# Kernel tuning notes

Measured on AMD Instinct MI355X. Metric: run time of the kernel, lower is better.

Reference implementation:

```python
import math
import jax, jax.numpy as jnp
import numpy as np

IN_FEATURES = 4096
OUT_FEATURES = 4096
BLOCK_SIZE = 256
N_TOKENS = 8192


def _butterfly_layout(out_blocks, in_blocks, butterfly_size):
    # sum of log2(n) butterfly factors with all-ones 2x2 twiddles:
    # block (o, i) is active iff o == i or o == i ^ 2^k for some factor k
    log_n = int(math.log2(butterfly_size))
    idx = np.arange(butterfly_size)
    layout = np.zeros((butterfly_size, butterfly_size), dtype=bool)
    layout[idx, idx] = True
    for k in range(log_n):
        layout[idx ^ (1 << k), idx] = True
    if out_blocks > butterfly_size:
        layout = np.tile(layout, (out_blocks // butterfly_size, 1))
    if in_blocks > butterfly_size:
        layout = np.tile(layout, (1, in_blocks // butterfly_size))
    return layout


def _flat_indices(layout):
    # For each output block, flat indices into [num_in_blocks * active_blocks_per_input]
    # selecting which per-input weight blocks are summed (embedding_bag mode='sum').
    num_out, num_in = layout.shape
    abpi = int(layout.sum(0)[0])
    abpo = int(layout.sum(1)[0])
    rank = np.cumsum(layout, axis=0) - 1  # rank of output o among active outputs of input i
    o_idx, i_idx = np.nonzero(layout)     # row-major -> grouped by output block
    flat = i_idx * abpi + rank[o_idx, i_idx]
    return flat.reshape(num_out, abpo).astype(np.int32), abpi


def setup_inputs() -> dict:
    key = jax.random.key(0)
    k1, k2 = jax.random.split(key)
    in_blocks = IN_FEATURES // BLOCK_SIZE
    out_blocks = OUT_FEATURES // BLOCK_SIZE
    butterfly_size = min(IN_FEATURES, OUT_FEATURES) // BLOCK_SIZE  # 16
    layout = _butterfly_layout(out_blocks, in_blocks, butterfly_size)
    flat_idx, abpi = _flat_indices(layout)  # abpi = log2(16)+1 = 5
    std = math.sqrt(2.0 / (5 * min(IN_FEATURES, OUT_FEATURES)))
    weight = jax.random.normal(k1, (IN_FEATURES, abpi, BLOCK_SIZE), dtype=jnp.float32) * std
    x = jax.random.normal(k2, (N_TOKENS, IN_FEATURES), dtype=jnp.float32)
    return {"x": x, "weight": weight, "flat_indices": jnp.asarray(flat_idx)}


def reference(x, weight, flat_indices):
    # x: [B, in_features]; weight: [in_features, abpi, block_size]
    in_features, abpi, bs = weight.shape
    num_in = in_features // bs
    B = x.shape[0]
    xb = x.reshape(B, num_in, bs)                  # [B, g, k]
    w = weight.reshape(num_in, bs, abpi, bs)       # [g, k, a, o]
    # per-input-block partial output blocks: [g, a, B, o]
    blocks = jnp.einsum('bgk,gkao->gabo', xb, w)
    blocks = blocks.reshape(num_in * abpi, B, bs)
    # gather + sum active blocks per output block (embedding_bag mode='sum')
    out_blocks = blocks[flat_indices].sum(axis=1)  # [num_out_blocks, B, bs]
    out = jnp.transpose(out_blocks, (1, 0, 2)).reshape(B, -1)  # [B, out_features]
    return out
```

## Files before the change

kernel.cpp:

```cpp
#include <hip/hip_runtime.h>
#include <stdint.h>

#define N_TOK 8192
#define IN_F 4096
#define OUT_F 4096
#define BS 256
#define ABPI 5
#define NFLAT 80

typedef __attribute__((ext_vector_type(8))) short short8;
typedef __attribute__((ext_vector_type(4))) float floatx4;
typedef __attribute__((ext_vector_type(4))) unsigned short ushort4v;
typedef __attribute__((ext_vector_type(8))) unsigned short ushort8v;

__device__ __forceinline__ unsigned short f2bf(float f) {
  union { float f; unsigned int u; } v; v.f = f;
  unsigned int r = v.u + 0x7FFFu + ((v.u >> 16) & 1u);
  return (unsigned short)(r >> 16);
}

__device__ __forceinline__ void async16(const void* g, void* l) {
  __builtin_amdgcn_global_load_lds((const __attribute__((address_space(1))) void*)g,
                                   (__attribute__((address_space(3))) void*)l, 16, 0, 0);
}

__global__ void cvt_x_kernel(const float4* __restrict__ x, ushort8v* __restrict__ xb) {
  int idx = blockIdx.x * 256 + threadIdx.x;
  float4 a = x[idx * 2], b = x[idx * 2 + 1];
  ushort8v o;
  o[0] = f2bf(a.x); o[1] = f2bf(a.y); o[2] = f2bf(a.z); o[3] = f2bf(a.w);
  o[4] = f2bf(b.x); o[5] = f2bf(b.y); o[6] = f2bf(b.z); o[7] = f2bf(b.w);
  xb[idx] = o;
}

__global__ void cvt_w_kernel(const float* __restrict__ w, unsigned short* __restrict__ wt) {
  __shared__ unsigned short tile[64][68];
  int b = blockIdx.x;
  int fi = b >> 4;
  int t  = b & 15;
  int k0 = (t >> 2) * 64, o0 = (t & 3) * 64;
  int g = fi / ABPI, a = fi % ABPI;
  int tid = threadIdx.x;
  int tr = tid >> 4, tc = tid & 15;
  #pragma unroll
  for (int i = 0; i < 4; ++i) {
    int k = k0 + i * 16 + tr;
    const float* src = w + (size_t)(g * 256 + k) * (ABPI * BS) + a * BS + o0 + tc * 4;
    float4 v = *(const float4*)src;
    tile[tc * 4 + 0][i * 16 + tr] = f2bf(v.x);
    tile[tc * 4 + 1][i * 16 + tr] = f2bf(v.y);
    tile[tc * 4 + 2][i * 16 + tr] = f2bf(v.z);
    tile[tc * 4 + 3][i * 16 + tr] = f2bf(v.w);
  }
  __syncthreads();
  #pragma unroll
  for (int i = 0; i < 4; ++i) {
    int o = i * 16 + tr;
    unsigned short* dst = wt + (size_t)fi * (BS * BS) + (size_t)(o0 + o) * BS + k0 + tc * 4;
    *(ushort4v*)dst = *(const ushort4v*)&tile[o][tc * 4];
  }
}

__global__ __launch_bounds__(256, 2)
void bfly_gemm(const unsigned short* __restrict__ xb,
               const unsigned short* __restrict__ wt,
               const int* __restrict__ fidx,
               float* __restrict__ out)
{
  __shared__ __align__(16) short As[128 * 64];
  __shared__ __align__(16) short Bs[128 * 64];

  const int tid = threadIdx.x;
  const int bx  = blockIdx.x;
  const int ob  = bx >> 7;
  const int rem = bx & 127;
  const int m0  = (rem >> 1) * 128;
  const int nh  = rem & 1;
  const int n0g = ob * 256 + nh * 128;

  int wbase[ABPI], gcol[ABPI];
  #pragma unroll
  for (int s = 0; s < ABPI; ++s) {
    int fi = fidx[ob * ABPI + s];
    wbase[s] = fi * (BS * BS);
    gcol[s]  = (fi / ABPI) * BS;
  }

  const int sr = tid >> 3;
  const int sc = tid & 7;
  const int lc = sc ^ (sr & 7);
  const size_t aBase = (size_t)(m0 + sr) * IN_F + lc * 8;
  const int    bBase = (nh * 128 + sr) * BS + lc * 8;
  short* aDst = As + tid * 8;
  short* bDst = Bs + tid * 8;

  const int lane = tid & 63;
  const int wv   = tid >> 6;
  const int wm   = (wv & 1) * 64;
  const int wn   = (wv >> 1) * 64;
  const int lrow = lane & 15;
  const int quad = lane >> 4;

  floatx4 acc[4][4] = {};

  for (int c = 0; c < 20; ++c) {
    const int s  = c >> 2;
    const int kk = (c & 3) * 64;
    const unsigned short* aG = xb + aBase + gcol[s] + kk;
    const unsigned short* bG = wt + wbase[s] + bBase + kk;
    __syncthreads();
    #pragma unroll
    for (int i = 0; i < 4; ++i) {
      async16(aG + (size_t)i * 32 * IN_F, aDst + i * 2048);
      async16(bG + i * 32 * BS,           bDst + i * 2048);
    }
    __syncthreads();
    #pragma unroll
    for (int ks = 0; ks < 2; ++ks) {
      short8 af[4], bf[4];
      const int ch = ((ks * 4 + quad) ^ (lrow & 7)) * 8;
      #pragma unroll
      for (int mt = 0; mt < 4; ++mt)
        af[mt] = *(const short8*)(As + (wm + mt * 16 + lrow) * 64 + ch);
      #pragma unroll
      for (int nt = 0; nt < 4; ++nt)
        bf[nt] = *(const short8*)(Bs + (wn + nt * 16 + lrow) * 64 + ch);
      #pragma unroll
      for (int mt = 0; mt < 4; ++mt)
        #pragma unroll
        for (int nt = 0; nt < 4; ++nt)
          acc[mt][nt] = __builtin_amdgcn_mfma_f32_16x16x32_bf16(af[mt], bf[nt], acc[mt][nt], 0, 0, 0);
    }
  }

  #pragma unroll
  for (int mt = 0; mt < 4; ++mt) {
    const int rbase = m0 + wm + mt * 16 + quad * 4;
    #pragma unroll
    for (int nt = 0; nt < 4; ++nt) {
      const int col = n0g + wn + nt * 16 + lrow;
      float* po = out + (size_t)rbase * OUT_F + col;
      #pragma unroll
      for (int r = 0; r < 4; ++r)
        po[(size_t)r * OUT_F] = acc[mt][nt][r];
    }
  }
}

extern "C" void kernel_launch(void* const* d_in, const int* in_sizes, int n_in,
                              void* d_out, int out_size, void* d_ws, size_t ws_size,
                              hipStream_t stream) {
  const float* x  = (const float*)d_in[0];
  const float* w  = (const float*)d_in[1];
  const int* fidx = (const int*)d_in[2];
  float* out = (float*)d_out;

  unsigned short* xb = (unsigned short*)d_ws;
  unsigned short* wt = xb + (size_t)N_TOK * IN_F;

  cvt_x_kernel<<<(N_TOK * IN_F) / (8 * 256), 256, 0, stream>>>((const float4*)x, (ushort8v*)xb);
  cvt_w_kernel<<<NFLAT * 16, 256, 0, stream>>>(w, wt);
  bfly_gemm<<<16 * 64 * 2, 256, 0, stream>>>(xb, wt, fidx, out);
}
```

Before: 355.6 us.

## Rewrite butterfly GEMM with 256x128 tiles and triple-buffered async LDS pipeline

Replaces the 128x128 single-buffered GEMM loop with a 512-thread, 256x128 tile kernel. It uses three LDS buffers in dynamic shared memory, filled by global_load_lds. Each k-tile is split into two phases that interleave the next tile's loads with fragment reads and MFMA work, using explicit waitcnt, sched_barrier and setprio. The intent is to hide global load latency and raise data reuse per block. It also adds a block-index swizzle for L2 locality and readfirstlane on the gathered indices. The cost is roughly 147KB of LDS per block, which limits occupancy to one block per CU, plus fragile hand-managed synchronisation.

```diff
diff --git a/kernel.cpp b/kernel.cpp
--- a/kernel.cpp
+++ b/kernel.cpp
@@ -61,27 +61,114 @@
   }
 }
 
-__global__ __launch_bounds__(256, 2)
+
+#define BM 256
+#define BN 128
+#define BK 64
+#define ABYTES 32768
+#define BBYTES 16384
+#define BUFBYTES 49152
+#define SMEM_TOTAL 147456
+
+__device__ __forceinline__ void ld_frags(const char* Ab, const char* Bb,
+                                         int rA, int rB, int c0, int c1, int mbyte, bool rdB,
+                                         short8 (&af)[4][2], short8 (&bfr)[2][2]) {
+  #pragma unroll
+  for (int m = 0; m < 4; ++m) {
+    const char* p = Ab + rA + mbyte + m * 2048;
+    af[m][0] = *(const short8*)(p + c0);
+    af[m][1] = *(const short8*)(p + c1);
+  }
+  if (rdB) {
+    #pragma unroll
+    for (int n = 0; n < 2; ++n) {
+      const char* p = Bb + rB + n * 2048;
+      bfr[n][0] = *(const short8*)(p + c0);
+      bfr[n][1] = *(const short8*)(p + c1);
+    }
+  }
+}
+
+__device__ __forceinline__ void mma_frags(int mbase, const short8 (&af)[4][2],
+                                          const short8 (&bfr)[2][2], floatx4 (&acc)[8][2]) {
+  #pragma unroll
+  for (int m = 0; m < 4; ++m)
+    #pragma unroll
+    for (int n = 0; n < 2; ++n) {
+      acc[mbase + m][n] = __builtin_amdgcn_mfma_f32_16x16x32_bf16(af[m][0], bfr[n][0], acc[mbase + m][n], 0, 0, 0);
+      acc[mbase + m][n] = __builtin_amdgcn_mfma_f32_16x16x32_bf16(af[m][1], bfr[n][1], acc[mbase + m][n], 0, 0, 0);
+    }
+}
+
+#define STAGE_PH0(uA, uB, Adst, Bdst)              \
+  do {                                             \
+    async16(pA0 + (uA), (Adst)         + tid16);   \
+    async16(pA1 + (uA), (Adst) +  8192 + tid16);   \
+    async16(pB0 + (uB), (Bdst)         + tid16);   \
+  } while (0)
+#define STAGE_PH1(uA, uB, Adst, Bdst)              \
+  do {                                             \
+    async16(pA2 + (uA), (Adst) + 16384 + tid16);   \
+    async16(pA3 + (uA), (Adst) + 24576 + tid16);   \
+    async16(pB1 + (uB), (Bdst) +  8192 + tid16);   \
+  } while (0)
+
+#define KTILE(u, Ab, Bb, Asd, Bsd, DOSTAGE, LASTWAIT)                       \
+  do {                                                                      \
+    int uA = 0, uB = 0;                                                     \
+    if (DOSTAGE) { int su = (u) >> 2, ku = ((u) & 3) * 64;                  \
+                   uA = gcol[su] + ku; uB = wbase[su] + ku; }               \
+    ld_frags(Ab, Bb, rA, rB, c0, c1, 0, true, af, bfr);                     \
+    if (DOSTAGE) STAGE_PH0(uA, uB, Asd, Bsd);                               \
+    __builtin_amdgcn_s_barrier();                                           \
+    asm volatile("s_waitcnt lgkmcnt(0)" ::: "memory");                      \
+    __builtin_amdgcn_sched_barrier(0);                                      \
+    __builtin_amdgcn_s_setprio(1);                                          \
+    mma_frags(0, af, bfr, acc);                                             \
+    __builtin_amdgcn_s_setprio(0);                                          \
+    __builtin_amdgcn_s_barrier();                                           \
+    ld_frags(Ab, Bb, rA, rB, c0, c1, 8192, false, af, bfr);                 \
+    if (DOSTAGE) STAGE_PH1(uA, uB, Asd, Bsd);                               \
+    __builtin_amdgcn_s_barrier();                                           \
+    asm volatile("s_waitcnt lgkmcnt(0)" ::: "memory");                      \
+    __builtin_amdgcn_sched_barrier(0);                                      \
+    __builtin_amdgcn_s_setprio(1);                                          \
+    mma_frags(4, af, bfr, acc);                                             \
+    __builtin_amdgcn_s_setprio(0);                                          \
+    if (DOSTAGE)       { asm volatile("s_waitcnt vmcnt(6)" ::: "memory");   \
+                         __builtin_amdgcn_sched_barrier(0); }               \
+    else if (LASTWAIT) { asm volatile("s_waitcnt vmcnt(0)" ::: "memory");   \
+                         __builtin_amdgcn_sched_barrier(0); }               \
+    __builtin_amdgcn_s_barrier();                                           \
+  } while (0)
+
+__global__ __launch_bounds__(512, 2)
 void bfly_gemm(const unsigned short* __restrict__ xb,
                const unsigned short* __restrict__ wt,
                const int* __restrict__ fidx,
                float* __restrict__ out)
 {
-  __shared__ __align__(16) short As[128 * 64];
-  __shared__ __align__(16) short Bs[128 * 64];
+  extern __shared__ __align__(16) char smem[];
+  char* const b0A = smem;
+  char* const b0B = b0A + ABYTES;
+  char* const b1A = smem + BUFBYTES;
+  char* const b1B = b1A + ABYTES;
+  char* const b2A = smem + 2 * BUFBYTES;
+  char* const b2B = b2A + ABYTES;
 
   const int tid = threadIdx.x;
   const int bx  = blockIdx.x;
-  const int ob  = bx >> 7;
-  const int rem = bx & 127;
-  const int m0  = (rem >> 1) * 128;
-  const int nh  = rem & 1;
+  const int swz = (bx & 7) * 128 + (bx >> 3);
+  const int ob  = swz >> 6;
+  const int mt  = (swz >> 1) & 31;
+  const int nh  = swz & 1;
+  const int m0  = mt * BM;
   const int n0g = ob * 256 + nh * 128;
 
   int wbase[ABPI], gcol[ABPI];
   #pragma unroll
   for (int s = 0; s < ABPI; ++s) {
-    int fi = fidx[ob * ABPI + s];
+    int fi = __builtin_amdgcn_readfirstlane(fidx[ob * ABPI + s]);
     wbase[s] = fi * (BS * BS);
     gcol[s]  = (fi / ABPI) * BS;
   }
@@ -89,60 +176,60 @@
   const int sr = tid >> 3;
   const int sc = tid & 7;
   const int lc = sc ^ (sr & 7);
-  const size_t aBase = (size_t)(m0 + sr) * IN_F + lc * 8;
-  const int    bBase = (nh * 128 + sr) * BS + lc * 8;
-  short* aDst = As + tid * 8;
-  short* bDst = Bs + tid * 8;
+  const int tid16 = tid * 16;
+  const unsigned short* pA0 = xb + (size_t)(m0 +   0 + sr) * IN_F + lc * 8;
+  const unsigned short* pA1 = xb + (size_t)(m0 +  64 + sr) * IN_F + lc * 8;
+  const unsigned short* pA2 = xb + (size_t)(m0 + 128 + sr) * IN_F + lc * 8;
+  const unsigned short* pA3 = xb + (size_t)(m0 + 192 + sr) * IN_F + lc * 8;
+  const unsigned short* pB0 = wt + (nh * 128 +  0 + sr) * BS + lc * 8;
+  const unsigned short* pB1 = wt + (nh * 128 + 64 + sr) * BS + lc * 8;
 
   const int lane = tid & 63;
   const int wv   = tid >> 6;
-  const int wm   = (wv & 1) * 64;
-  const int wn   = (wv >> 1) * 64;
+  const int wm   = (wv >> 2) * 128;
+  const int wn   = (wv & 3) * 32;
   const int lrow = lane & 15;
   const int quad = lane >> 4;
-
-  floatx4 acc[4][4] = {};
-
-  for (int c = 0; c < 20; ++c) {
-    const int s  = c >> 2;
-    const int kk = (c & 3) * 64;
-    const unsigned short* aG = xb + aBase + gcol[s] + kk;
-    const unsigned short* bG = wt + wbase[s] + bBase + kk;
-    __syncthreads();
+  const int rA = (wm + lrow) * 128;
+  const int rB = (wn + lrow) * 128;
+  const int c0 = ((quad)     ^ (lrow & 7)) * 16;
+  const int c1 = ((quad + 4) ^ (lrow & 7)) * 16;
+
+  short8 af[4][2], bfr[2][2];
+  floatx4 acc[8][2] = {};
+
+  {
+    const int uA0 = gcol[0], uB0 = wbase[0];
+    STAGE_PH0(uA0, uB0, b0A, b0B);
+    STAGE_PH1(uA0, uB0, b0A, b0B);
+    __builtin_amdgcn_sched_barrier(0);
+    STAGE_PH0(uA0 + 64, uB0 + 64, b1A, b1B);
+    STAGE_PH1(uA0 + 64, uB0 + 64, b1A, b1B);
+    asm volatile("s_waitcnt vmcnt(6)" ::: "memory");
+    __builtin_amdgcn_sched_barrier(0);
+    __builtin_amdgcn_s_barrier();
+  }
+
+  #pragma unroll 1
+  for (int j = 0; j < 6; ++j) {
+    const int t = j * 3;
+    KTILE(t + 2, b0A, b0B, b2A, b2B, true, false);
+    KTILE(t + 3, b1A, b1B, b0A, b0B, true, false);
+    KTILE(t + 4, b2A, b2B, b1A, b1B, true, false);
+  }
+  KTILE(0, b0A, b0B, b0A, b0B, false, true);
+  KTILE(0, b1A, b1B, b0A, b0B, false, false);
+
+  #pragma unroll
+  for (int m = 0; m < 8; ++m) {
+    const int row = m0 + wm + m * 16 + quad * 4;
     #pragma unroll
-    for (int i = 0; i < 4; ++i) {
-      async16(aG + (size_t)i * 32 * IN_F, aDst + i * 2048);
-      async16(bG + i * 32 * BS,           bDst + i * 2048);
-    }
-    __syncthreads();
-    #pragma unroll
-    for (int ks = 0; ks < 2; ++ks) {
-      short8 af[4], bf[4];
-      const int ch = ((ks * 4 + quad) ^ (lrow & 7)) * 8;
-      #pragma unroll
-      for (int mt = 0; mt < 4; ++mt)
-        af[mt] = *(const short8*)(As + (wm + mt * 16 + lrow) * 64 + ch);
-      #pragma unroll
-      for (int nt = 0; nt < 4; ++nt)
-        bf[nt] = *(const short8*)(Bs + (wn + nt * 16 + lrow) * 64 + ch);
-      #pragma unroll
-      for (int mt = 0; mt < 4; ++mt)
-        #pragma unroll
-        for (int nt = 0; nt < 4; ++nt)
-          acc[mt][nt] = __builtin_amdgcn_mfma_f32_16x16x32_bf16(af[mt], bf[nt], acc[mt][nt], 0, 0, 0);
-    }
-  }
-
-  #pragma unroll
-  for (int mt = 0; mt < 4; ++mt) {
-    const int rbase = m0 + wm + mt * 16 + quad * 4;
-    #pragma unroll
-    for (int nt = 0; nt < 4; ++nt) {
-      const int col = n0g + wn + nt * 16 + lrow;
-      float* po = out + (size_t)rbase * OUT_F + col;
+    for (int n = 0; n < 2; ++n) {
+      const int col = n0g + wn + n * 16 + lrow;
+      float* po = out + (size_t)row * OUT_F + col;
       #pragma unroll
       for (int r = 0; r < 4; ++r)
-        po[(size_t)r * OUT_F] = acc[mt][nt][r];
+        po[(size_t)r * OUT_F] = acc[m][n][r];
     }
   }
 }
@@ -158,7 +245,14 @@
   unsigned short* xb = (unsigned short*)d_ws;
   unsigned short* wt = xb + (size_t)N_TOK * IN_F;
 
+  static int smem_set = 0;
+  if (!smem_set) {
+    hipFuncSetAttribute((const void*)bfly_gemm,
+                        hipFuncAttributeMaxDynamicSharedMemorySize, SMEM_TOTAL);
+    smem_set = 1;
+  }
+
   cvt_x_kernel<<<(N_TOK * IN_F) / (8 * 256), 256, 0, stream>>>((const float4*)x, (ushort8v*)xb);
   cvt_w_kernel<<<NFLAT * 16, 256, 0, stream>>>(w, wt);
-  bfly_gemm<<<16 * 64 * 2, 256, 0, stream>>>(xb, wt, fidx, out);
-}
+  bfly_gemm<<<16 * 32 * 2, 512, SMEM_TOTAL, stream>>>(xb, wt, fidx, out);
+}
```

New measurement: 333.3 us. 6.3% less time.

## Rewrite butterfly GEMM as 256x256 double-buffered, phase-interleaved MFMA kernel

Applied to the files above, without the earlier changes.

Replaces the 128x128 single-buffered GEMM with a 256x256 tile per 512-thread block. It double-buffers A and B in 128KB of dynamic LDS and splits each K tile into four phases that interleave async global-to-LDS loads with MFMA work, using explicit vmcnt waits and s_setprio. It also swizzles the block index for L2 locality and makes the weight-index loads wave-uniform with readfirstlane. The aim is to hide load latency and raise reuse per loaded byte. In exchange it uses far more registers and LDS, which limits occupancy, and the hand-tuned barrier and waitcnt scheme is fragile.

```diff
diff --git a/kernel.cpp b/kernel.cpp
--- a/kernel.cpp
+++ b/kernel.cpp
@@ -61,27 +61,117 @@
   }
 }
 
-__global__ __launch_bounds__(256, 2)
+
+#define BM 256
+#define BN 256
+#define BK 64
+#define ABYTES 32768
+#define BUFBYTES 65536
+#define SMEM_TOTAL 131072
+
+__device__ __forceinline__ void ld_half_A(const char* p, int c0, int c1, short8 (&af)[4][2]) {
+  #pragma unroll
+  for (int mt = 0; mt < 4; ++mt) {
+    const char* q = p + mt * 2048;
+    af[mt][0] = *(const short8*)(q + c0);
+    af[mt][1] = *(const short8*)(q + c1);
+  }
+}
+
+__device__ __forceinline__ void ld_pair_B(const char* p, int c0, int c1, short8 (&bf)[2][2]) {
+  #pragma unroll
+  for (int nt = 0; nt < 2; ++nt) {
+    const char* q = p + nt * 2048;
+    bf[nt][0] = *(const short8*)(q + c0);
+    bf[nt][1] = *(const short8*)(q + c1);
+  }
+}
+
+__device__ __forceinline__ void mma16(const short8 (&af)[4][2], const short8 (&bf)[2][2],
+                                      floatx4 (&acc)[8][4], int mb, int nb) {
+  #pragma unroll
+  for (int mt = 0; mt < 4; ++mt)
+    #pragma unroll
+    for (int nt = 0; nt < 2; ++nt) {
+      acc[mb + mt][nb + nt] =
+          __builtin_amdgcn_mfma_f32_16x16x32_bf16(af[mt][0], bf[nt][0], acc[mb + mt][nb + nt], 0, 0, 0);
+      acc[mb + mt][nb + nt] =
+          __builtin_amdgcn_mfma_f32_16x16x32_bf16(af[mt][1], bf[nt][1], acc[mb + mt][nb + nt], 0, 0, 0);
+    }
+}
+
+#define PH_OPEN                                            \
+  __builtin_amdgcn_s_barrier();                            \
+  asm volatile("s_waitcnt lgkmcnt(0)" ::: "memory");       \
+  __builtin_amdgcn_sched_barrier(0);                       \
+  __builtin_amdgcn_s_setprio(1)
+
+#define KTILE(tt, Ab, Bb, Asd, Bsd, DOSTAGE, LAST)                              \
+  do {                                                                          \
+    int uA = 0, uB = 0;                                                         \
+    if (DOSTAGE) { const int u = (tt) + 1, su = u >> 2, ku = (u & 3) * 64;      \
+                   uA = gcol[su] + ku; uB = wbase[su] + ku; }                   \
+                                                \
+    ld_half_A((Ab) + rAb, c0, c1, af);                                          \
+    ld_pair_B((Bb) + rBb, c0, c1, bf01);                                        \
+    if (DOSTAGE) { async16(pA0 + uA, (Asd)         + tid16);                    \
+                   async16(pA2 + uA, (Asd) + 16384 + tid16);                    \
+                   async16(pB0 + uB, (Bsd)         + tid16);                    \
+                   async16(pB1 + uB, (Bsd) +  8192 + tid16); }                  \
+    PH_OPEN; mma16(af, bf01, acc, 0, 0);                                        \
+    __builtin_amdgcn_s_setprio(0);                                              \
+    __builtin_amdgcn_s_barrier();                                               \
+                                                \
+    ld_pair_B((Bb) + rBb + 4096, c0, c1, bf23);                                 \
+    if (DOSTAGE) { async16(pB2 + uB, (Bsd) + 16384 + tid16);                    \
+                   async16(pB3 + uB, (Bsd) + 24576 + tid16); }                  \
+    PH_OPEN; mma16(af, bf23, acc, 0, 2);                                        \
+    __builtin_amdgcn_s_setprio(0);                                              \
+    if (DOSTAGE)   { asm volatile("s_waitcnt vmcnt(6)" ::: "memory");           \
+                     __builtin_amdgcn_sched_barrier(0); }                       \
+    else if (LAST) { asm volatile("s_waitcnt vmcnt(0)" ::: "memory");           \
+                     __builtin_amdgcn_sched_barrier(0); }                       \
+    __builtin_amdgcn_s_barrier();                                               \
+                                                \
+    ld_half_A((Ab) + rAb + 8192, c0, c1, af);                                   \
+    if (DOSTAGE) { async16(pA1 + uA, (Asd) +  8192 + tid16);                    \
+                   async16(pA3 + uA, (Asd) + 24576 + tid16); }                  \
+    PH_OPEN; mma16(af, bf23, acc, 4, 2);                                        \
+    __builtin_amdgcn_s_setprio(0);                                              \
+    __builtin_amdgcn_s_barrier();                                               \
+                          \
+    __builtin_amdgcn_s_setprio(1);                                              \
+    mma16(af, bf01, acc, 4, 0);                                                 \
+    __builtin_amdgcn_s_setprio(0);                                              \
+    if (DOSTAGE) { asm volatile("s_waitcnt vmcnt(2)" ::: "memory");             \
+                   __builtin_amdgcn_sched_barrier(0); }                         \
+    __builtin_amdgcn_s_barrier();                                               \
+  } while (0)
+
+__global__ __launch_bounds__(512, 2)
 void bfly_gemm(const unsigned short* __restrict__ xb,
                const unsigned short* __restrict__ wt,
                const int* __restrict__ fidx,
                float* __restrict__ out)
 {
-  __shared__ __align__(16) short As[128 * 64];
-  __shared__ __align__(16) short Bs[128 * 64];
+  extern __shared__ __align__(16) char smem[];
+  char* const b0A = smem;
+  char* const b0B = b0A + ABYTES;
+  char* const b1A = smem + BUFBYTES;
+  char* const b1B = b1A + ABYTES;
 
   const int tid = threadIdx.x;
   const int bx  = blockIdx.x;
-  const int ob  = bx >> 7;
-  const int rem = bx & 127;
-  const int m0  = (rem >> 1) * 128;
-  const int nh  = rem & 1;
-  const int n0g = ob * 256 + nh * 128;
+  const int swz = (bx & 7) * 64 + (bx >> 3);
+  const int ob  = swz >> 5;
+  const int mt0 = swz & 31;
+  const int m0  = mt0 * BM;
+  const int n0g = ob * 256;
 
   int wbase[ABPI], gcol[ABPI];
   #pragma unroll
   for (int s = 0; s < ABPI; ++s) {
-    int fi = fidx[ob * ABPI + s];
+    int fi = __builtin_amdgcn_readfirstlane(fidx[ob * ABPI + s]);
     wbase[s] = fi * (BS * BS);
     gcol[s]  = (fi / ABPI) * BS;
   }
@@ -89,60 +179,64 @@
   const int sr = tid >> 3;
   const int sc = tid & 7;
   const int lc = sc ^ (sr & 7);
-  const size_t aBase = (size_t)(m0 + sr) * IN_F + lc * 8;
-  const int    bBase = (nh * 128 + sr) * BS + lc * 8;
-  short* aDst = As + tid * 8;
-  short* bDst = Bs + tid * 8;
+  const int tid16 = tid * 16;
+  const unsigned short* pA0 = xb + (size_t)(m0 +   0 + sr) * IN_F + lc * 8;
+  const unsigned short* pA1 = xb + (size_t)(m0 +  64 + sr) * IN_F + lc * 8;
+  const unsigned short* pA2 = xb + (size_t)(m0 + 128 + sr) * IN_F + lc * 8;
+  const unsigned short* pA3 = xb + (size_t)(m0 + 192 + sr) * IN_F + lc * 8;
+  const unsigned short* pB0 = wt + (  0 + sr) * BS + lc * 8;
+  const unsigned short* pB1 = wt + ( 64 + sr) * BS + lc * 8;
+  const unsigned short* pB2 = wt + (128 + sr) * BS + lc * 8;
+  const unsigned short* pB3 = wt + (192 + sr) * BS + lc * 8;
 
   const int lane = tid & 63;
   const int wv   = tid >> 6;
-  const int wm   = (wv & 1) * 64;
-  const int wn   = (wv >> 1) * 64;
+  const int wm   = (wv >> 2) * 128;
+  const int wn   = (wv & 3) * 64;
   const int lrow = lane & 15;
   const int quad = lane >> 4;
-
-  floatx4 acc[4][4] = {};
-
-  for (int c = 0; c < 20; ++c) {
-    const int s  = c >> 2;
-    const int kk = (c & 3) * 64;
-    const unsigned short* aG = xb + aBase + gcol[s] + kk;
-    const unsigned short* bG = wt + wbase[s] + bBase + kk;
-    __syncthreads();
+  const int rAb  = (wm + lrow) * 128;
+  const int rBb  = (wn + lrow) * 128;
+  const int c0   = ((quad)     ^ (lrow & 7)) * 16;
+  const int c1   = ((quad + 4) ^ (lrow & 7)) * 16;
+
+  short8 af[4][2], bf01[2][2], bf23[2][2];
+  floatx4 acc[8][4] = {};
+
+  {
+    const int uA0 = gcol[0], uB0 = wbase[0];
+    async16(pA0 + uA0, b0A         + tid16);
+    async16(pA1 + uA0, b0A +  8192 + tid16);
+    async16(pA2 + uA0, b0A + 16384 + tid16);
+    async16(pA3 + uA0, b0A + 24576 + tid16);
+    async16(pB0 + uB0, b0B         + tid16);
+    async16(pB1 + uB0, b0B +  8192 + tid16);
+    async16(pB2 + uB0, b0B + 16384 + tid16);
+    async16(pB3 + uB0, b0B + 24576 + tid16);
+    asm volatile("s_waitcnt vmcnt(0)" ::: "memory");
+    __builtin_amdgcn_sched_barrier(0);
+    __builtin_amdgcn_s_barrier();
+  }
+
+  #pragma unroll 1
+  for (int j = 0; j < 9; ++j) {
+    const int t = j * 2;
+    KTILE(t,     b0A, b0B, b1A, b1B, true, false);
+    KTILE(t + 1, b1A, b1B, b0A, b0B, true, false);
+  }
+  KTILE(18, b0A, b0B, b1A, b1B, true, false);
+  KTILE(19, b1A, b1B, b0A, b0B, false, true);
+
+  #pragma unroll
+  for (int m = 0; m < 8; ++m) {
+    const int row = m0 + wm + (m >> 2) * 64 + (m & 3) * 16 + quad * 4;
     #pragma unroll
-    for (int i = 0; i < 4; ++i) {
-      async16(aG + (size_t)i * 32 * IN_F, aDst + i * 2048);
-      async16(bG + i * 32 * BS,           bDst + i * 2048);
-    }
-    __syncthreads();
-    #pragma unroll
-    for (int ks = 0; ks < 2; ++ks) {
-      short8 af[4], bf[4];
-      const int ch = ((ks * 4 + quad) ^ (lrow & 7)) * 8;
-      #pragma unroll
-      for (int mt = 0; mt < 4; ++mt)
-        af[mt] = *(const short8*)(As + (wm + mt * 16 + lrow) * 64 + ch);
-      #pragma unroll
-      for (int nt = 0; nt < 4; ++nt)
-        bf[nt] = *(const short8*)(Bs + (wn + nt * 16 + lrow) * 64 + ch);
-      #pragma unroll
-      for (int mt = 0; mt < 4; ++mt)
-        #pragma unroll
-        for (int nt = 0; nt < 4; ++nt)
-          acc[mt][nt] = __builtin_amdgcn_mfma_f32_16x16x32_bf16(af[mt], bf[nt], acc[mt][nt], 0, 0, 0);
-    }
-  }
-
-  #pragma unroll
-  for (int mt = 0; mt < 4; ++mt) {
-    const int rbase = m0 + wm + mt * 16 + quad * 4;
-    #pragma unroll
-    for (int nt = 0; nt < 4; ++nt) {
-      const int col = n0g + wn + nt * 16 + lrow;
-      float* po = out + (size_t)rbase * OUT_F + col;
+    for (int n = 0; n < 4; ++n) {
+      const int col = n0g + wn + n * 16 + lrow;
+      float* po = out + (size_t)row * OUT_F + col;
       #pragma unroll
       for (int r = 0; r < 4; ++r)
-        po[(size_t)r * OUT_F] = acc[mt][nt][r];
+        po[(size_t)r * OUT_F] = acc[m][n][r];
     }
   }
 }
@@ -158,7 +252,14 @@
   unsigned short* xb = (unsigned short*)d_ws;
   unsigned short* wt = xb + (size_t)N_TOK * IN_F;
 
+  static int smem_set = 0;
+  if (!smem_set) {
+    hipFuncSetAttribute((const void*)bfly_gemm,
+                        hipFuncAttributeMaxDynamicSharedMemorySize, SMEM_TOTAL);
+    smem_set = 1;
+  }
+
   cvt_x_kernel<<<(N_TOK * IN_F) / (8 * 256), 256, 0, stream>>>((const float4*)x, (ushort8v*)xb);
   cvt_w_kernel<<<NFLAT * 16, 256, 0, stream>>>(w, wt);
-  bfly_gemm<<<16 * 64 * 2, 256, 0, stream>>>(xb, wt, fidx, out);
-}
+  bfly_gemm<<<16 * 32, 512, SMEM_TOTAL, stream>>>(xb, wt, fidx, out);
+}
```

Measured after the change: 323.6 us. 9.0% less time.
